# Kernel tuning notes

Measured on AMD Instinct MI355X. Metric: run time of the kernel, lower is better.

Reference implementation:

```python
import jax, jax.numpy as jnp
import numpy as np

B, N, DIN, D, E, STEP = 4, 1024, 256, 256, 5, 5


def setup_inputs() -> dict:
    key = jax.random.key(0)
    ks = jax.random.split(key, 14)
    s = 0.02  # weight init scale
    inp = {
        "node_features": jax.random.normal(ks[0], (B, N, DIN), dtype=jnp.float32),
        # dense per-edge-type adjacency; scaled so messages stay in a sane range
        "adj_matrices": jax.random.uniform(ks[1], (B, E, N, N), dtype=jnp.float32) * (2.0 / N),
        "fc_in_w": jax.random.normal(ks[2], (D, DIN), dtype=jnp.float32) * s,
        "fc_in_b": jnp.zeros((D,), dtype=jnp.float32),
        "edge_w": jax.random.normal(ks[3], (E, D, D), dtype=jnp.float32) * s,
        "edge_b": jax.random.normal(ks[4], (E, D), dtype=jnp.float32) * s,
        "gru_w_ih": jax.random.normal(ks[5], (3 * D, D), dtype=jnp.float32) * s,
        "gru_w_hh": jax.random.normal(ks[6], (3 * D, D), dtype=jnp.float32) * s,
        "gru_b_ih": jnp.zeros((3 * D,), dtype=jnp.float32),
        "gru_b_hh": jnp.zeros((3 * D,), dtype=jnp.float32),
        "conv1_w": jax.random.normal(ks[7], (D, D), dtype=jnp.float32) * s,
        "conv1_b": jnp.zeros((D,), dtype=jnp.float32),
        "conv2_w": jax.random.normal(ks[8], (D, D), dtype=jnp.float32) * s,
        "conv2_b": jnp.zeros((D,), dtype=jnp.float32),
    }
    return inp


def _gru_cell(x, h, w_ih, w_hh, b_ih, b_hh):
    # torch GRUCell: gates ordered [r, z, n]
    gi = x @ w_ih.T + b_ih  # [B*N, 3D]
    gh = h @ w_hh.T + b_hh
    ir, iz, inn = jnp.split(gi, 3, axis=-1)
    hr, hz, hn = jnp.split(gh, 3, axis=-1)
    r = jax.nn.sigmoid(ir + hr)
    z = jax.nn.sigmoid(iz + hz)
    n = jnp.tanh(inn + r * hn)
    return (1.0 - z) * n + z * h


def reference(node_features, adj_matrices, fc_in_w, fc_in_b, edge_w, edge_b,
              gru_w_ih, gru_w_hh, gru_b_ih, gru_b_hh,
              conv1_w, conv1_b, conv2_w, conv2_b):
    h = node_features @ fc_in_w.T + fc_in_b  # [B, N, D]
    sum_edge_b = jnp.sum(edge_b, axis=0)  # accumulated biases over edge types
    for _ in range(STEP):
        # messages per edge type: adj_e @ h  -> [B, E, N, D]
        msgs = jnp.einsum('benm,bmd->bend', adj_matrices, h)
        # per-edge-type linear (y = x @ W_e.T) then accumulate over edge types
        acc = jnp.einsum('bend,ekd->bnk', msgs, edge_w) + sum_edge_b  # [B, N, D]
        h = _gru_cell(acc, h, gru_w_ih, gru_w_hh, gru_b_ih, gru_b_hh)
    node_states = h  # [B, N, D]
    # conv1d with kernel_size=1 over node axis == per-node linear on channels
    attn_weights = jax.nn.sigmoid(node_states @ conv1_w.T + conv1_b)  # [B, N, D]
    feats = jnp.tanh(node_states @ conv2_w.T + conv2_b)  # [B, N, D]
    graph_embedding = jnp.sum(attn_weights * feats, axis=1)  # sum over nodes -> [B, D]
    attn_map = jnp.mean(attn_weights, axis=2)  # mean over channels -> [B, N]
    return (graph_embedding, node_states, attn_map)
```

## Files before the change

kernel.cpp:

```cpp
#include <hip/hip_runtime.h>
#include <hip/hip_bf16.h>
#include <cstdint>


typedef __attribute__((ext_vector_type(8))) short bf16x8;
typedef __attribute__((ext_vector_type(4))) float f32x4;

__device__ __forceinline__ float bf2f(__hip_bfloat16 x) { return __bfloat162float(x); }
__device__ __forceinline__ __hip_bfloat16 f2bf(float x) { return __float2bfloat16(x); }
__device__ __forceinline__ short f2bs(float x) {
  __hip_bfloat16 h = __float2bfloat16(x);
  return *reinterpret_cast<short*>(&h);
}
__device__ __forceinline__ float s2f(short x) {
  __hip_bfloat16 h = *reinterpret_cast<__hip_bfloat16*>(&x);
  return __bfloat162float(h);
}

__device__ __forceinline__ bf16x8 ld8_ext(const void* base, long off, bool f32) {
  if (f32) {
    const float* p = (const float*)base + off;
    bf16x8 r;
#pragma unroll
    for (int i = 0; i < 8; ++i) r[i] = f2bs(p[i]);
    return r;
  }
  return *(const bf16x8*)((const __hip_bfloat16*)base + off);
}

__device__ __forceinline__ bf16x8 ld8_sum5(const __hip_bfloat16* part, int row, int k) {
  const long base = (long)row * 256 + (long)(row >> 10) * 1048576 + k;
  float s[8] = {0.f, 0.f, 0.f, 0.f, 0.f, 0.f, 0.f, 0.f};
#pragma unroll
  for (int e = 0; e < 5; ++e) {
    bf16x8 v = *(const bf16x8*)(part + base + e * 262144);
#pragma unroll
    for (int j = 0; j < 8; ++j) s[j] += s2f(v[j]);
  }
  bf16x8 r;
#pragma unroll
  for (int j = 0; j < 8; ++j) r[j] = f2bs(s[j]);
  return r;
}

__global__ void detect_dtype(const uint32_t* __restrict__ raw, int* __restrict__ flag) {
  __shared__ int cnt;
  if (threadIdx.x == 0) cnt = 0;
  __syncthreads();
  int c = 0;
  for (int i = threadIdx.x; i < 512; i += 256) {
    uint32_t byte = (raw[i] >> 8) & 0xFF;
    if (byte >= 0x28 && byte <= 0x40) ++c;
  }
  atomicAdd(&cnt, c);
  __syncthreads();
  if (threadIdx.x == 0) *flag = (cnt < 300) ? 1 : 0;
}

__global__ void prep_pool(const void* fcb, const void* bih, const void* bhh,
                          const void* c1b, const void* c2b, const void* edgeb,
                          const int* __restrict__ flag,
                          float* __restrict__ pool, float* __restrict__ ge,
                          float* __restrict__ am32) {
  const bool f32 = (*flag != 0);
  for (int t = threadIdx.x; t < 2560; t += 256) {
    const void* p; int i;
    if (t < 256)       { p = fcb;  i = t; }
    else if (t < 1024) { p = bih;  i = t - 256; }
    else if (t < 1792) { p = bhh;  i = t - 1024; }
    else if (t < 2048) { p = c1b;  i = t - 1792; }
    else if (t < 2304) { p = c2b;  i = t - 2048; }
    else {
      int k = t - 2304; float s = 0.f;
      for (int e = 0; e < 5; ++e)
        s += f32 ? ((const float*)edgeb)[e * 256 + k]
                 : bf2f(((const __hip_bfloat16*)edgeb)[e * 256 + k]);
      pool[t] = s; continue;
    }
    pool[t] = f32 ? ((const float*)p)[i] : bf2f(((const __hip_bfloat16*)p)[i]);
  }
  for (int t = threadIdx.x; t < 1024; t += 256) ge[t] = 0.f;
  for (int t = threadIdx.x; t < 4096; t += 256) am32[t] = 0.f;
}

__global__ void bias_gi_k(const float* __restrict__ pool,
                          const __hip_bfloat16* __restrict__ wih,
                          float* __restrict__ out) {
  const int n = blockIdx.x * 256 + threadIdx.x;
  if (n >= 768) return;
  float s = pool[256 + n];
  for (int k = 0; k < 256; ++k) s += pool[2304 + k] * bf2f(wih[n * 256 + k]);
  out[n] = s;
}

__global__ void wcvt_all(const void* fcw, const void* edw, const void* wih,
                         const void* whh, const void* c1w, const void* c2w,
                         const int* __restrict__ flag, __hip_bfloat16* __restrict__ dst) {
  const bool f32 = (*flag != 0);
  const int i = blockIdx.x * 256 + threadIdx.x;
  const void* src; int off;
  if      (i < 65536)  { src = fcw; off = i; }
  else if (i < 393216) { src = edw; off = i - 65536; }
  else if (i < 589824) { src = wih; off = i - 393216; }
  else if (i < 786432) { src = whh; off = i - 589824; }
  else if (i < 851968) { src = c1w; off = i - 786432; }
  else                 { src = c2w; off = i - 851968; }
  dst[i] = f32 ? f2bf(((const float*)src)[off])
               : ((const __hip_bfloat16*)src)[off];
}

__global__ void adj_cvt(const void* __restrict__ src, const int* __restrict__ flag,
                        __hip_bfloat16* __restrict__ dst) {
  const bool f32 = (*flag != 0);
  const long i = ((long)blockIdx.x * 256 + threadIdx.x) * 8;
  bf16x8 r;
  if (f32) {
    const float* p = (const float*)src + i;
#pragma unroll
    for (int j = 0; j < 8; ++j) r[j] = f2bs(p[j]);
  } else {
    r = *(const bf16x8*)((const __hip_bfloat16*)src + i);
  }
  *(bf16x8*)(dst + i) = r;
}

template<bool HAS_BIAS, bool DUAL>
__global__ __launch_bounds__(256)
void gemm_bt128(const __hip_bfloat16* __restrict__ A, const __hip_bfloat16* __restrict__ Bt,
                const float* __restrict__ bias, __hip_bfloat16* __restrict__ C,
                const __hip_bfloat16* __restrict__ A2, const __hip_bfloat16* __restrict__ Bt2,
                const float* __restrict__ bias2, __hip_bfloat16* __restrict__ C2,
                int K, int lda, int ldb, int ldc,
                long aBatch, int zdivA, int zmodA,
                long bBatch, int zdivB, int zmodB,
                long cBatch, int zdivC, int zSplit)
{
  __shared__ __align__(16) __hip_bfloat16 sA[128 * 64];
  __shared__ __align__(16) __hip_bfloat16 sB[64 * 64];
  const int t = threadIdx.x;
  const int w = t >> 6;
  const int l = t & 63;
  const int m0 = blockIdx.x * 128;
  const int n0 = blockIdx.y * 64;
  int z = blockIdx.z;

  const __hip_bfloat16* Au = A; const __hip_bfloat16* Btu = Bt;
  const float* biasu = bias; __hip_bfloat16* Cu = C;
  if (DUAL && z >= zSplit) { Au = A2; Btu = Bt2; biasu = bias2; Cu = C2; z -= zSplit; }

  const __hip_bfloat16* Ab = Au + (long)((z / zdivA) % zmodA) * aBatch;
  const __hip_bfloat16* Bb = Btu + (long)((z / zdivB) % zmodB) * bBatch;

  int sra[4], sca[4];
#pragma unroll
  for (int i = 0; i < 4; ++i) {
    const int p = t + 256 * i;
    sra[i] = p >> 3;
    sca[i] = (p & 7) ^ (sra[i] & 7);
  }
  const int p0 = t, p1 = t + 256;
  const int sr0 = p0 >> 3, sc0 = (p0 & 7) ^ (sr0 & 7);
  const int sr1 = p1 >> 3, sc1 = (p1 & 7) ^ (sr1 & 7);

  f32x4 acc[2][4];
#pragma unroll
  for (int i = 0; i < 2; ++i)
#pragma unroll
    for (int j = 0; j < 4; ++j) acc[i][j] = (f32x4){0.f, 0.f, 0.f, 0.f};

  const int r15 = l & 15;
  const int quad = l >> 4;

  for (int k0 = 0; k0 < K; k0 += 64) {
    bf16x8 av[4];
#pragma unroll
    for (int i = 0; i < 4; ++i)
      av[i] = *(const bf16x8*)(Ab + (long)(m0 + sra[i]) * lda + (k0 + sca[i] * 8));
    bf16x8 b0 = *(const bf16x8*)(Bb + (long)(n0 + sr0) * ldb + (k0 + sc0 * 8));
    bf16x8 b1 = *(const bf16x8*)(Bb + (long)(n0 + sr1) * ldb + (k0 + sc1 * 8));
    __syncthreads();
#pragma unroll
    for (int i = 0; i < 4; ++i) *(bf16x8*)(sA + (t + 256 * i) * 8) = av[i];
    *(bf16x8*)(sB + p0 * 8) = b0;
    *(bf16x8*)(sB + p1 * 8) = b1;
    __syncthreads();
#pragma unroll
    for (int ks = 0; ks < 2; ++ks) {
      const int cg = ks * 4 + quad;
      bf16x8 aF[2], bF[4];
#pragma unroll
      for (int mi = 0; mi < 2; ++mi) {
        const int row = mi * 64 + w * 16 + r15;
        aF[mi] = *(const bf16x8*)(sA + row * 64 + ((cg ^ (row & 7)) * 8));
      }
#pragma unroll
      for (int ni = 0; ni < 4; ++ni) {
        const int nrow = ni * 16 + r15;
        bF[ni] = *(const bf16x8*)(sB + nrow * 64 + ((cg ^ (nrow & 7)) * 8));
      }
#pragma unroll
      for (int mi = 0; mi < 2; ++mi)
#pragma unroll
        for (int ni = 0; ni < 4; ++ni)
          acc[mi][ni] = __builtin_amdgcn_mfma_f32_16x16x32_bf16(
              aF[mi], bF[ni], acc[mi][ni], 0, 0, 0);
    }
  }

  const long cOff = (long)(z / zdivC) * cBatch;
#pragma unroll
  for (int mi = 0; mi < 2; ++mi) {
#pragma unroll
    for (int ni = 0; ni < 4; ++ni) {
      const int n = n0 + ni * 16 + r15;
      float bv = 0.f;
      if (HAS_BIAS) bv = biasu[n];
#pragma unroll
      for (int r = 0; r < 4; ++r) {
        const int m = m0 + mi * 64 + w * 16 + quad * 4 + r;
        Cu[cOff + (long)m * ldc + n] = f2bf(acc[mi][ni][r] + bv);
      }
    }
  }
}

__global__ __launch_bounds__(256)
void part_gh(const __hip_bfloat16* __restrict__ adjb,
             const __hip_bfloat16* __restrict__ heT,
             __hip_bfloat16* __restrict__ part,
             const __hip_bfloat16* __restrict__ hbf,
             const __hip_bfloat16* __restrict__ whh,
             const float* __restrict__ bhh,
             __hip_bfloat16* __restrict__ gh)
{
  __shared__ __align__(16) __hip_bfloat16 sA[128 * 64];
  __shared__ __align__(16) __hip_bfloat16 sB[64 * 64];
  const int t = threadIdx.x;
  const int w = t >> 6;
  const int l = t & 63;
  const int bid = blockIdx.x;

  const __hip_bfloat16* Ab; const __hip_bfloat16* Bb;
  __hip_bfloat16* Cu; const float* biasu = nullptr;
  int K, lda, ldb, ldc, m0, n0;
  bool has_bias;
  if (bid < 640) {
    const int z = bid >> 5, rem = bid & 31;
    m0 = (rem & 7) * 128; n0 = (rem >> 3) * 64;
    Ab = adjb + (long)z * 1048576; lda = 1024; K = 1024;
    Bb = heT + (long)z * 262144;  ldb = 1024;
    Cu = part + (long)z * 262144; ldc = 256;
    has_bias = false;
  } else {
    const int idx = bid - 640;
    m0 = (idx & 31) * 128; n0 = (idx >> 5) * 64;
    Ab = hbf; lda = 256; K = 256;
    Bb = whh; ldb = 256;
    Cu = gh;  ldc = 768;
    biasu = bhh; has_bias = true;
  }

  int sra[4], sca[4];
#pragma unroll
  for (int i = 0; i < 4; ++i) {
    const int p = t + 256 * i;
    sra[i] = p >> 3;
    sca[i] = (p & 7) ^ (sra[i] & 7);
  }
  const int p0 = t, p1 = t + 256;
  const int sr0 = p0 >> 3, sc0 = (p0 & 7) ^ (sr0 & 7);
  const int sr1 = p1 >> 3, sc1 = (p1 & 7) ^ (sr1 & 7);

  f32x4 acc[2][4];
#pragma unroll
  for (int i = 0; i < 2; ++i)
#pragma unroll
    for (int j = 0; j < 4; ++j) acc[i][j] = (f32x4){0.f, 0.f, 0.f, 0.f};

  const int r15 = l & 15;
  const int quad = l >> 4;

  for (int k0 = 0; k0 < K; k0 += 64) {
    bf16x8 av[4];
#pragma unroll
    for (int i = 0; i < 4; ++i)
      av[i] = *(const bf16x8*)(Ab + (long)(m0 + sra[i]) * lda + (k0 + sca[i] * 8));
    bf16x8 b0 = *(const bf16x8*)(Bb + (long)(n0 + sr0) * ldb + (k0 + sc0 * 8));
    bf16x8 b1 = *(const bf16x8*)(Bb + (long)(n0 + sr1) * ldb + (k0 + sc1 * 8));
    __syncthreads();
#pragma unroll
    for (int i = 0; i < 4; ++i) *(bf16x8*)(sA + (t + 256 * i) * 8) = av[i];
    *(bf16x8*)(sB + p0 * 8) = b0;
    *(bf16x8*)(sB + p1 * 8) = b1;
    __syncthreads();
#pragma unroll
    for (int ks = 0; ks < 2; ++ks) {
      const int cg = ks * 4 + quad;
      bf16x8 aF[2], bF[4];
#pragma unroll
      for (int mi = 0; mi < 2; ++mi) {
        const int row = mi * 64 + w * 16 + r15;
        aF[mi] = *(const bf16x8*)(sA + row * 64 + ((cg ^ (row & 7)) * 8));
      }
#pragma unroll
      for (int ni = 0; ni < 4; ++ni) {
        const int nrow = ni * 16 + r15;
        bF[ni] = *(const bf16x8*)(sB + nrow * 64 + ((cg ^ (nrow & 7)) * 8));
      }
#pragma unroll
      for (int mi = 0; mi < 2; ++mi)
#pragma unroll
        for (int ni = 0; ni < 4; ++ni)
          acc[mi][ni] = __builtin_amdgcn_mfma_f32_16x16x32_bf16(
              aF[mi], bF[ni], acc[mi][ni], 0, 0, 0);
    }
  }

#pragma unroll
  for (int mi = 0; mi < 2; ++mi) {
#pragma unroll
    for (int ni = 0; ni < 4; ++ni) {
      const int n = n0 + ni * 16 + r15;
      const float bv = has_bias ? biasu[n] : 0.f;
#pragma unroll
      for (int r = 0; r < 4; ++r) {
        const int m = m0 + mi * 64 + w * 16 + quad * 4 + r;
        Cu[(long)m * ldc + n] = f2bf(acc[mi][ni][r] + bv);
      }
    }
  }
}

__global__ __launch_bounds__(256)
void gi_gate(const __hip_bfloat16* __restrict__ part,
             const __hip_bfloat16* __restrict__ wih,
             const float* __restrict__ biasgi,
             const __hip_bfloat16* __restrict__ gh,
             __hip_bfloat16* __restrict__ hbf,
             void* __restrict__ ns_out, const int* __restrict__ flag)
{
  __shared__ __align__(16) __hip_bfloat16 sA[64 * 64];
  __shared__ __align__(16) __hip_bfloat16 sB0[64 * 64];
  __shared__ __align__(16) __hip_bfloat16 sB1[64 * 64];
  __shared__ __align__(16) __hip_bfloat16 sB2[64 * 64];
  const int t = threadIdx.x;
  const int w = t >> 6;
  const int l = t & 63;
  const int m0 = (blockIdx.x & 63) * 64;
  const int n0 = (blockIdx.x >> 6) * 64;

  const int p0 = t, p1 = t + 256;
  const int sr0 = p0 >> 3, sc0 = (p0 & 7) ^ (sr0 & 7);
  const int sr1 = p1 >> 3, sc1 = (p1 & 7) ^ (sr1 & 7);

  f32x4 acc[3][4];
#pragma unroll
  for (int g = 0; g < 3; ++g)
#pragma unroll
    for (int j = 0; j < 4; ++j) acc[g][j] = (f32x4){0.f, 0.f, 0.f, 0.f};

  const int mrow = w * 16 + (l & 15);
  const int r15 = l & 15;
  const int quad = l >> 4;

  for (int k0 = 0; k0 < 256; k0 += 64) {
    bf16x8 a0 = ld8_sum5(part, m0 + sr0, k0 + sc0 * 8);
    bf16x8 a1 = ld8_sum5(part, m0 + sr1, k0 + sc1 * 8);
    bf16x8 bg[3][2];
#pragma unroll
    for (int g = 0; g < 3; ++g) {
      bg[g][0] = *(const bf16x8*)(wih + (long)(g * 256 + n0 + sr0) * 256 + (k0 + sc0 * 8));
      bg[g][1] = *(const bf16x8*)(wih + (long)(g * 256 + n0 + sr1) * 256 + (k0 + sc1 * 8));
    }
    __syncthreads();
    *(bf16x8*)(sA + p0 * 8) = a0;
    *(bf16x8*)(sA + p1 * 8) = a1;
    *(bf16x8*)(sB0 + p0 * 8) = bg[0][0]; *(bf16x8*)(sB0 + p1 * 8) = bg[0][1];
    *(bf16x8*)(sB1 + p0 * 8) = bg[1][0]; *(bf16x8*)(sB1 + p1 * 8) = bg[1][1];
    *(bf16x8*)(sB2 + p0 * 8) = bg[2][0]; *(bf16x8*)(sB2 + p1 * 8) = bg[2][1];
    __syncthreads();
#pragma unroll
    for (int ks = 0; ks < 2; ++ks) {
      const int cg = ks * 4 + quad;
      bf16x8 af = *(const bf16x8*)(sA + mrow * 64 + ((cg ^ (mrow & 7)) * 8));
#pragma unroll
      for (int t4 = 0; t4 < 4; ++t4) {
        const int nrow = t4 * 16 + r15;
        const int so = nrow * 64 + ((cg ^ (nrow & 7)) * 8);
        bf16x8 b0f = *(const bf16x8*)(sB0 + so);
        bf16x8 b1f = *(const bf16x8*)(sB1 + so);
        bf16x8 b2f = *(const bf16x8*)(sB2 + so);
        acc[0][t4] = __builtin_amdgcn_mfma_f32_16x16x32_bf16(af, b0f, acc[0][t4], 0, 0, 0);
        acc[1][t4] = __builtin_amdgcn_mfma_f32_16x16x32_bf16(af, b1f, acc[1][t4], 0, 0, 0);
        acc[2][t4] = __builtin_amdgcn_mfma_f32_16x16x32_bf16(af, b2f, acc[2][t4], 0, 0, 0);
      }
    }
  }

  const bool f32out = ns_out && (*flag != 0);
#pragma unroll
  for (int t4 = 0; t4 < 4; ++t4) {
    const int n = n0 + t4 * 16 + r15;
    const float bgr = biasgi[n];
    const float bgz = biasgi[256 + n];
    const float bgn = biasgi[512 + n];
#pragma unroll
    for (int r = 0; r < 4; ++r) {
      const int m = m0 + w * 16 + quad * 4 + r;
      const long gb = (long)m * 768;
      const float ir = acc[0][t4][r] + bgr;
      const float iz = acc[1][t4][r] + bgz;
      const float inn = acc[2][t4][r] + bgn;
      const float hr = bf2f(gh[gb + n]);
      const float hz = bf2f(gh[gb + 256 + n]);
      const float hn = bf2f(gh[gb + 512 + n]);
      const long hidx = (long)m * 256 + n;
      const float h = bf2f(hbf[hidx]);
      const float rr = 1.f / (1.f + __expf(-(ir + hr)));
      const float zz = 1.f / (1.f + __expf(-(iz + hz)));
      const float nn = tanhf(inn + rr * hn);
      const float hnew = (1.f - zz) * nn + zz * h;
      const __hip_bfloat16 hb = f2bf(hnew);
      hbf[hidx] = hb;
      if (ns_out) {
        if (f32out) ((float*)ns_out)[1024 + hidx] = hnew;
        else        ((__hip_bfloat16*)ns_out)[1024 + hidx] = hb;
      }
    }
  }
}

template<int OUT_MODE, bool HAS_BIAS, int A_MODE, bool DUAL>
__global__ __launch_bounds__(256)
void gemm_bt(const void* __restrict__ A, const __hip_bfloat16* __restrict__ Bt,
             const float* __restrict__ bias, void* __restrict__ Cp,
             const void* __restrict__ A2, const __hip_bfloat16* __restrict__ Bt2,
             const float* __restrict__ bias2, void* __restrict__ Cp2,
             const int* __restrict__ flag,
             int Kg, int ngrp, int lda, int ldb, int ldc,
             long aBatch, int zdivA, int zmodA,
             long bBatch, int zdivB, int zmodB,
             long cBatch, int zdivC, long aGrp, long bGrp, int zSplit)
{
  __shared__ __align__(16) __hip_bfloat16 sA[64 * 64];
  __shared__ __align__(16) __hip_bfloat16 sB[64 * 64];
  const bool af32 = (A_MODE == 1) ? (*flag != 0) : false;
  const int t = threadIdx.x;
  const int w = t >> 6;
  const int l = t & 63;
  const int m0 = blockIdx.x * 64;
  const int n0 = blockIdx.y * 64;
  int z = blockIdx.z;

  const void* Au = A; const __hip_bfloat16* Btu = Bt;
  const float* biasu = bias; void* Cpu = Cp;
  bool second = false;
  if (DUAL && z >= zSplit) {
    Au = A2; Btu = Bt2; biasu = bias2; Cpu = Cp2; z -= zSplit; second = true;
  }

  const long aOff = (long)((z / zdivA) % zmodA) * aBatch;
  const __hip_bfloat16* Bb = Btu + (long)((z / zdivB) % zmodB) * bBatch;

  const int p0 = t, p1 = t + 256;
  const int sr0 = p0 >> 3, sc0 = (p0 & 7) ^ (sr0 & 7);
  const int sr1 = p1 >> 3, sc1 = (p1 & 7) ^ (sr1 & 7);

  f32x4 acc[4];
#pragma unroll
  for (int i = 0; i < 4; ++i) acc[i] = (f32x4){0.f, 0.f, 0.f, 0.f};

  const int mrow = w * 16 + (l & 15);
  const int quad = l >> 4;

  for (int g = 0; g < ngrp; ++g) {
    const long aG = aOff + (long)g * aGrp;
    const __hip_bfloat16* Bg = Bb + (long)g * bGrp;
    for (int k0 = 0; k0 < Kg; k0 += 64) {
      bf16x8 a0, a1;
      if (A_MODE == 2 && !second) {
        a0 = ld8_sum5((const __hip_bfloat16*)Au, m0 + sr0, k0 + sc0 * 8);
        a1 = ld8_sum5((const __hip_bfloat16*)Au, m0 + sr1, k0 + sc1 * 8);
      } else if (A_MODE == 1) {
        a0 = ld8_ext(Au, aG + (long)(m0 + sr0) * lda + (k0 + sc0 * 8), af32);
        a1 = ld8_ext(Au, aG + (long)(m0 + sr1) * lda + (k0 + sc1 * 8), af32);
      } else {
        const __hip_bfloat16* Ab = (const __hip_bfloat16*)Au;
        a0 = *(const bf16x8*)(Ab + aG + (long)(m0 + sr0) * lda + (k0 + sc0 * 8));
        a1 = *(const bf16x8*)(Ab + aG + (long)(m0 + sr1) * lda + (k0 + sc1 * 8));
      }
      bf16x8 b0 = *(const bf16x8*)(Bg + (long)(n0 + sr0) * ldb + (k0 + sc0 * 8));
      bf16x8 b1 = *(const bf16x8*)(Bg + (long)(n0 + sr1) * ldb + (k0 + sc1 * 8));
      __syncthreads();
      *(bf16x8*)(sA + p0 * 8) = a0;
      *(bf16x8*)(sA + p1 * 8) = a1;
      *(bf16x8*)(sB + p0 * 8) = b0;
      *(bf16x8*)(sB + p1 * 8) = b1;
      __syncthreads();
#pragma unroll
      for (int ks = 0; ks < 2; ++ks) {
        const int cg = ks * 4 + quad;
        bf16x8 af = *(const bf16x8*)(sA + mrow * 64 + ((cg ^ (mrow & 7)) * 8));
#pragma unroll
        for (int t4 = 0; t4 < 4; ++t4) {
          const int nrow = t4 * 16 + (l & 15);
          bf16x8 bfr = *(const bf16x8*)(sB + nrow * 64 + ((cg ^ (nrow & 7)) * 8));
          acc[t4] = __builtin_amdgcn_mfma_f32_16x16x32_bf16(af, bfr, acc[t4], 0, 0, 0);
        }
      }
    }
  }

  const long cOff = (long)(z / zdivC) * cBatch;
#pragma unroll
  for (int t4 = 0; t4 < 4; ++t4) {
    const int n = n0 + t4 * 16 + (l & 15);
    float bv = 0.f;
    if (HAS_BIAS) bv = biasu[n];
#pragma unroll
    for (int r = 0; r < 4; ++r) {
      const int m = m0 + w * 16 + quad * 4 + r;
      const float v = acc[t4][r] + bv;
      if (OUT_MODE == 0)
        ((__hip_bfloat16*)Cpu)[cOff + (long)m * ldc + n] = f2bf(v);
      else
        ((float*)Cpu)[cOff + (long)m * ldc + n] = v;
    }
  }
}

__global__ void gru_gate8(const __hip_bfloat16* __restrict__ gi,
                          const __hip_bfloat16* __restrict__ gh,
                          __hip_bfloat16* __restrict__ hbf,
                          void* __restrict__ ns_out, const int* __restrict__ flag)
{
  const int t = blockIdx.x * 256 + threadIdx.x;
  const int m = t >> 5;
  const int k = (t & 31) * 8;
  const long gb = (long)m * 768 + k;
  bf16x8 vir = *(const bf16x8*)(gi + gb);
  bf16x8 viz = *(const bf16x8*)(gi + gb + 256);
  bf16x8 vin = *(const bf16x8*)(gi + gb + 512);
  bf16x8 vhr = *(const bf16x8*)(gh + gb);
  bf16x8 vhz = *(const bf16x8*)(gh + gb + 256);
  bf16x8 vhn = *(const bf16x8*)(gh + gb + 512);
  const long hidx = (long)m * 256 + k;
  bf16x8 vh = *(const bf16x8*)(hbf + hidx);
  bf16x8 out;
  float hf[8];
#pragma unroll
  for (int j = 0; j < 8; ++j) {
    const float r = 1.f / (1.f + __expf(-(s2f(vir[j]) + s2f(vhr[j]))));
    const float zz = 1.f / (1.f + __expf(-(s2f(viz[j]) + s2f(vhz[j]))));
    const float nn = tanhf(s2f(vin[j]) + r * s2f(vhn[j]));
    hf[j] = (1.f - zz) * nn + zz * s2f(vh[j]);
    out[j] = f2bs(hf[j]);
  }
  *(bf16x8*)(hbf + hidx) = out;
  if (ns_out) {
    if (*flag) {
      float* o = (float*)ns_out + 1024 + hidx;
#pragma unroll
      for (int j = 0; j < 8; ++j) o[j] = hf[j];
    } else {
      *(bf16x8*)((__hip_bfloat16*)ns_out + 1024 + hidx) = out;
    }
  }
}

__global__ __launch_bounds__(256)
void conv_fused(const __hip_bfloat16* __restrict__ hbf,
                const __hip_bfloat16* __restrict__ c1w,
                const __hip_bfloat16* __restrict__ c2w,
                const float* __restrict__ pool,
                float* __restrict__ geg, float* __restrict__ am32)
{
  __shared__ __align__(16) __hip_bfloat16 sA[64 * 64];
  __shared__ __align__(16) __hip_bfloat16 sB1[64 * 64];
  __shared__ __align__(16) __hip_bfloat16 sB2[64 * 64];
  __shared__ float sge[64];
  __shared__ float sam[64];
  const int t = threadIdx.x, w = t >> 6, l = t & 63;
  const int m0 = blockIdx.x * 64, n0 = blockIdx.y * 64;
  if (t < 64) { sge[t] = 0.f; sam[t] = 0.f; }
  const int p0 = t, p1 = t + 256;
  const int sr0 = p0 >> 3, sc0 = (p0 & 7) ^ (sr0 & 7);
  const int sr1 = p1 >> 3, sc1 = (p1 & 7) ^ (sr1 & 7);
  f32x4 a1[4], a2[4];
#pragma unroll
  for (int i = 0; i < 4; ++i) { a1[i] = (f32x4){0,0,0,0}; a2[i] = (f32x4){0,0,0,0}; }
  const int mrow = w * 16 + (l & 15);
  const int quad = l >> 4;
  for (int k0 = 0; k0 < 256; k0 += 64) {
    bf16x8 va0 = *(const bf16x8*)(hbf + (long)(m0 + sr0) * 256 + (k0 + sc0 * 8));
    bf16x8 va1 = *(const bf16x8*)(hbf + (long)(m0 + sr1) * 256 + (k0 + sc1 * 8));
    bf16x8 vb0 = *(const bf16x8*)(c1w + (long)(n0 + sr0) * 256 + (k0 + sc0 * 8));
    bf16x8 vb1 = *(const bf16x8*)(c1w + (long)(n0 + sr1) * 256 + (k0 + sc1 * 8));
    bf16x8 vc0 = *(const bf16x8*)(c2w + (long)(n0 + sr0) * 256 + (k0 + sc0 * 8));
    bf16x8 vc1 = *(const bf16x8*)(c2w + (long)(n0 + sr1) * 256 + (k0 + sc1 * 8));
    __syncthreads();
    *(bf16x8*)(sA + p0 * 8) = va0;  *(bf16x8*)(sA + p1 * 8) = va1;
    *(bf16x8*)(sB1 + p0 * 8) = vb0; *(bf16x8*)(sB1 + p1 * 8) = vb1;
    *(bf16x8*)(sB2 + p0 * 8) = vc0; *(bf16x8*)(sB2 + p1 * 8) = vc1;
    __syncthreads();
#pragma unroll
    for (int ks = 0; ks < 2; ++ks) {
      const int cg = ks * 4 + quad;
      bf16x8 af = *(const bf16x8*)(sA + mrow * 64 + ((cg ^ (mrow & 7)) * 8));
#pragma unroll
      for (int t4 = 0; t4 < 4; ++t4) {
        const int nrow = t4 * 16 + (l & 15);
        bf16x8 b1f = *(const bf16x8*)(sB1 + nrow * 64 + ((cg ^ (nrow & 7)) * 8));
        bf16x8 b2f = *(const bf16x8*)(sB2 + nrow * 64 + ((cg ^ (nrow & 7)) * 8));
        a1[t4] = __builtin_amdgcn_mfma_f32_16x16x32_bf16(af, b1f, a1[t4], 0, 0, 0);
        a2[t4] = __builtin_amdgcn_mfma_f32_16x16x32_bf16(af, b2f, a2[t4], 0, 0, 0);
      }
    }
  }
  float asum[4] = {0.f, 0.f, 0.f, 0.f};
#pragma unroll
  for (int t4 = 0; t4 < 4; ++t4) {
    const int n = n0 + t4 * 16 + (l & 15);
    const float bb1 = pool[1792 + n], bb2 = pool[2048 + n];
    float g = 0.f;
#pragma unroll
    for (int r = 0; r < 4; ++r) {
      const float av = 1.f / (1.f + __expf(-(a1[t4][r] + bb1)));
      const float fv = tanhf(a2[t4][r] + bb2);
      g += av * fv;
      asum[r] += av;
    }
    atomicAdd(&sge[t4 * 16 + (l & 15)], g);
  }
#pragma unroll
  for (int r = 0; r < 4; ++r) atomicAdd(&sam[w * 16 + quad * 4 + r], asum[r]);
  __syncthreads();
  if (t < 64) atomicAdd(&geg[(m0 >> 10) * 256 + n0 + t], sge[t]);
  else if (t < 128) atomicAdd(&am32[m0 + (t - 64)], sam[t - 64]);
}

__global__ void finish_out(const float* __restrict__ ge, const float* __restrict__ am32,
                           void* __restrict__ dout, const int* __restrict__ flag)
{
  const int t = blockIdx.x * 256 + threadIdx.x;
  const bool f32 = (*flag != 0);
  if (t < 1024) {
    if (f32) ((float*)dout)[t] = ge[t];
    else     ((__hip_bfloat16*)dout)[t] = f2bf(ge[t]);
  } else {
    const float v = am32[t - 1024] * (1.f / 256.f);
    if (f32) ((float*)dout)[1049600 + t - 1024] = v;
    else     ((__hip_bfloat16*)dout)[1049600 + t - 1024] = f2bf(v);
  }
}

extern "C" void kernel_launch(void* const* d_in, const int* in_sizes, int n_in,
                              void* d_out, int out_size, void* d_ws, size_t ws_size,
                              hipStream_t stream) {
  (void)in_sizes; (void)n_in; (void)out_size;
  const void* node_f = d_in[0];
  const void* adj    = d_in[1];
  const void* fc_w   = d_in[2];
  const void* fc_b   = d_in[3];
  const void* edge_w = d_in[4];
  const void* edge_b = d_in[5];
  const void* w_ih   = d_in[6];
  const void* w_hh   = d_in[7];
  const void* b_ih   = d_in[8];
  const void* b_hh   = d_in[9];
  const void* c1w    = d_in[10];
  const void* c1b    = d_in[11];
  const void* c2w    = d_in[12];
  const void* c2b    = d_in[13];

  char* ws = (char*)d_ws;
  const size_t MB = (size_t)1 << 20;
  int*            flag = (int*)(ws);
  float*          bp   = (float*)(ws + 256);
  float*          ge   = (float*)(ws + 14336);
  float*          am32 = (float*)(ws + 18432);
  __hip_bfloat16* wbf  = (__hip_bfloat16*)(ws + 34816);
  __hip_bfloat16* hbf  = (__hip_bfloat16*)(ws + 1869824);
  char*           S    = ws + 3966976;
  __hip_bfloat16* heT  = (__hip_bfloat16*)(S);
  __hip_bfloat16* part = (__hip_bfloat16*)(S + 10 * MB);
  __hip_bfloat16* gi   = (__hip_bfloat16*)(S + 20 * MB);
  __hip_bfloat16* gh   = (__hip_bfloat16*)(S + 26 * MB);
  __hip_bfloat16* adjb = (__hip_bfloat16*)(ws + 40 * MB);

  const bool has_split = ws_size >= 38 * MB;
  const bool has_adjb  = ws_size >= 81 * MB;

  detect_dtype<<<1, 256, 0, stream>>>((const uint32_t*)adj, flag);
  prep_pool<<<1, 256, 0, stream>>>(fc_b, b_ih, b_hh, c1b, c2b, edge_b, flag, bp, ge, am32);
  wcvt_all<<<3584, 256, 0, stream>>>(fc_w, edge_w, w_ih, w_hh, c1w, c2w, flag, wbf);
  bias_gi_k<<<3, 256, 0, stream>>>(bp, wbf + 393216, bp + 2560);
  if (has_adjb) adj_cvt<<<10240, 256, 0, stream>>>(adj, flag, adjb);

  gemm_bt<0, true, 1, false><<<dim3(64, 4, 1), 256, 0, stream>>>(
      node_f, wbf + 0, bp + 0, hbf, nullptr, nullptr, nullptr, nullptr, flag,
      256, 1, 256, 256, 256, 0, 1, 1, 0, 1, 1, 0, 1, 0, 0, 0);

  for (int s = 0; s < 5; ++s) {
    if (has_adjb) {
      gemm_bt128<false, false><<<dim3(2, 16, 20), 256, 0, stream>>>(
          wbf + 65536, hbf, nullptr, heT, nullptr, nullptr, nullptr, nullptr,
          256, 256, 256, 1024,
          65536, 1, 5,
          262144, 5, 4,
          262144, 1, 0);
      part_gh<<<1024, 256, 0, stream>>>(adjb, heT, part,
                                        hbf, wbf + 589824, bp + 1024, gh);
      gi_gate<<<256, 256, 0, stream>>>(part, wbf + 393216, bp + 2560, gh, hbf,
                                       (s == 4) ? d_out : nullptr, flag);
    } else if (has_split) {
      gemm_bt<0, false, 0, false><<<dim3(4, 16, 20), 256, 0, stream>>>(
          wbf + 65536, hbf, nullptr, heT, nullptr, nullptr, nullptr, nullptr, flag,
          256, 1, 256, 256, 1024,
          65536, 1, 5, 262144, 5, 4,
          262144, 1, 0, 0, 0);
      gemm_bt<0, false, 1, false><<<dim3(16, 4, 20), 256, 0, stream>>>(
          adj, heT, nullptr, part, nullptr, nullptr, nullptr, nullptr, flag,
          1024, 1, 1024, 1024, 256,
          1048576, 1, 20, 262144, 1, 20,
          262144, 1, 0, 0, 0);
      gemm_bt<0, true, 2, true><<<dim3(64, 12, 2), 256, 0, stream>>>(
          part, wbf + 393216, bp + 2560, gi,
          hbf,  wbf + 589824, bp + 1024, gh, flag,
          256, 1, 256, 256, 768, 0, 1, 1, 0, 1, 1, 0, 1, 0, 0, 1);
      gru_gate8<<<512, 256, 0, stream>>>(gi, gh, hbf,
                                         (s == 4) ? d_out : nullptr, flag);
    } else {
      gemm_bt<0, false, 0, false><<<dim3(4, 16, 20), 256, 0, stream>>>(
          wbf + 65536, hbf, nullptr, heT, nullptr, nullptr, nullptr, nullptr, flag,
          256, 1, 256, 256, 1024,
          65536, 1, 5, 262144, 5, 4,
          262144, 1, 0, 0, 0);
      gemm_bt<0, true, 1, false><<<dim3(16, 4, 4), 256, 0, stream>>>(
          adj, heT, bp + 2304, part, nullptr, nullptr, nullptr, nullptr, flag,
          1024, 5, 1024, 1024, 256,
          (long)5 * 1048576, 1, 4, (long)5 * 262144, 1, 4,
          262144, 1, 1048576, 262144, 0);
      gemm_bt<0, true, 0, true><<<dim3(64, 12, 2), 256, 0, stream>>>(
          part, wbf + 393216, bp + 256, gi,
          hbf,  wbf + 589824, bp + 1024, gh, flag,
          256, 1, 256, 256, 768, 0, 1, 1, 0, 1, 1, 0, 1, 0, 0, 1);
      gru_gate8<<<512, 256, 0, stream>>>(gi, gh, hbf,
                                         (s == 4) ? d_out : nullptr, flag);
    }
  }

  conv_fused<<<dim3(64, 4), 256, 0, stream>>>(hbf, wbf + 786432, wbf + 851968,
                                              bp, ge, am32);
  finish_out<<<20, 256, 0, stream>>>(ge, am32, d_out, flag);
}
```

Before: 432.8 us.

## Fold edge weights into GRU input weights and drop per-step edge GEMM

Reassociates the message path: instead of computing h@W_e^T per edge type each step, the code multiplies adjacency by h directly (msgs per edge) and folds W_ih into the edge weights once up front (V_e = W_ih·W_e), so the GRU input GEMM consumes all five edge messages over a K of 1280. This removes one GEMM launch per step and writes a transposed copy of h from the gate epilogue so the adjacency GEMM can read it directly. In exchange the gi GEMM has five times larger K and the adjacency GEMM output buffer now holds per-edge messages. A simple register prefetch of the next k-tile is added to the gi loop.

```diff
diff --git a/kernel.cpp b/kernel.cpp
--- a/kernel.cpp
+++ b/kernel.cpp
@@ -95,9 +95,21 @@
 
 __global__ void wcvt_all(const void* fcw, const void* edw, const void* wih,
                          const void* whh, const void* c1w, const void* c2w,
-                         const int* __restrict__ flag, __hip_bfloat16* __restrict__ dst) {
+                         const int* __restrict__ flag, __hip_bfloat16* __restrict__ dst,
+                         __hip_bfloat16* __restrict__ ewT) {
   const bool f32 = (*flag != 0);
   const int i = blockIdx.x * 256 + threadIdx.x;
+  if (i >= 917504) {
+    if (!ewT) return;
+    const int j = i - 917504;
+    const int e = j >> 16;
+    const int r = j & 65535;
+    const int d = r >> 8, k = r & 255;
+    const int off = e * 65536 + k * 256 + d;
+    ewT[j] = f32 ? f2bf(((const float*)edw)[off])
+                 : ((const __hip_bfloat16*)edw)[off];
+    return;
+  }
   const void* src; int off;
   if      (i < 65536)  { src = fcw; off = i; }
   else if (i < 393216) { src = edw; off = i - 65536; }
@@ -124,114 +136,14 @@
   *(bf16x8*)(dst + i) = r;
 }
 
-template<bool HAS_BIAS, bool DUAL>
 __global__ __launch_bounds__(256)
-void gemm_bt128(const __hip_bfloat16* __restrict__ A, const __hip_bfloat16* __restrict__ Bt,
-                const float* __restrict__ bias, __hip_bfloat16* __restrict__ C,
-                const __hip_bfloat16* __restrict__ A2, const __hip_bfloat16* __restrict__ Bt2,
-                const float* __restrict__ bias2, __hip_bfloat16* __restrict__ C2,
-                int K, int lda, int ldb, int ldc,
-                long aBatch, int zdivA, int zmodA,
-                long bBatch, int zdivB, int zmodB,
-                long cBatch, int zdivC, int zSplit)
-{
-  __shared__ __align__(16) __hip_bfloat16 sA[128 * 64];
-  __shared__ __align__(16) __hip_bfloat16 sB[64 * 64];
-  const int t = threadIdx.x;
-  const int w = t >> 6;
-  const int l = t & 63;
-  const int m0 = blockIdx.x * 128;
-  const int n0 = blockIdx.y * 64;
-  int z = blockIdx.z;
-
-  const __hip_bfloat16* Au = A; const __hip_bfloat16* Btu = Bt;
-  const float* biasu = bias; __hip_bfloat16* Cu = C;
-  if (DUAL && z >= zSplit) { Au = A2; Btu = Bt2; biasu = bias2; Cu = C2; z -= zSplit; }
-
-  const __hip_bfloat16* Ab = Au + (long)((z / zdivA) % zmodA) * aBatch;
-  const __hip_bfloat16* Bb = Btu + (long)((z / zdivB) % zmodB) * bBatch;
-
-  int sra[4], sca[4];
-#pragma unroll
-  for (int i = 0; i < 4; ++i) {
-    const int p = t + 256 * i;
-    sra[i] = p >> 3;
-    sca[i] = (p & 7) ^ (sra[i] & 7);
-  }
-  const int p0 = t, p1 = t + 256;
-  const int sr0 = p0 >> 3, sc0 = (p0 & 7) ^ (sr0 & 7);
-  const int sr1 = p1 >> 3, sc1 = (p1 & 7) ^ (sr1 & 7);
-
-  f32x4 acc[2][4];
-#pragma unroll
-  for (int i = 0; i < 2; ++i)
-#pragma unroll
-    for (int j = 0; j < 4; ++j) acc[i][j] = (f32x4){0.f, 0.f, 0.f, 0.f};
-
-  const int r15 = l & 15;
-  const int quad = l >> 4;
-
-  for (int k0 = 0; k0 < K; k0 += 64) {
-    bf16x8 av[4];
-#pragma unroll
-    for (int i = 0; i < 4; ++i)
-      av[i] = *(const bf16x8*)(Ab + (long)(m0 + sra[i]) * lda + (k0 + sca[i] * 8));
-    bf16x8 b0 = *(const bf16x8*)(Bb + (long)(n0 + sr0) * ldb + (k0 + sc0 * 8));
-    bf16x8 b1 = *(const bf16x8*)(Bb + (long)(n0 + sr1) * ldb + (k0 + sc1 * 8));
-    __syncthreads();
-#pragma unroll
-    for (int i = 0; i < 4; ++i) *(bf16x8*)(sA + (t + 256 * i) * 8) = av[i];
-    *(bf16x8*)(sB + p0 * 8) = b0;
-    *(bf16x8*)(sB + p1 * 8) = b1;
-    __syncthreads();
-#pragma unroll
-    for (int ks = 0; ks < 2; ++ks) {
-      const int cg = ks * 4 + quad;
-      bf16x8 aF[2], bF[4];
-#pragma unroll
-      for (int mi = 0; mi < 2; ++mi) {
-        const int row = mi * 64 + w * 16 + r15;
-        aF[mi] = *(const bf16x8*)(sA + row * 64 + ((cg ^ (row & 7)) * 8));
-      }
-#pragma unroll
-      for (int ni = 0; ni < 4; ++ni) {
-        const int nrow = ni * 16 + r15;
-        bF[ni] = *(const bf16x8*)(sB + nrow * 64 + ((cg ^ (nrow & 7)) * 8));
-      }
-#pragma unroll
-      for (int mi = 0; mi < 2; ++mi)
-#pragma unroll
-        for (int ni = 0; ni < 4; ++ni)
-          acc[mi][ni] = __builtin_amdgcn_mfma_f32_16x16x32_bf16(
-              aF[mi], bF[ni], acc[mi][ni], 0, 0, 0);
-    }
-  }
-
-  const long cOff = (long)(z / zdivC) * cBatch;
-#pragma unroll
-  for (int mi = 0; mi < 2; ++mi) {
-#pragma unroll
-    for (int ni = 0; ni < 4; ++ni) {
-      const int n = n0 + ni * 16 + r15;
-      float bv = 0.f;
-      if (HAS_BIAS) bv = biasu[n];
-#pragma unroll
-      for (int r = 0; r < 4; ++r) {
-        const int m = m0 + mi * 64 + w * 16 + quad * 4 + r;
-        Cu[cOff + (long)m * ldc + n] = f2bf(acc[mi][ni][r] + bv);
-      }
-    }
-  }
-}
-
-__global__ __launch_bounds__(256)
-void part_gh(const __hip_bfloat16* __restrict__ adjb,
-             const __hip_bfloat16* __restrict__ heT,
-             __hip_bfloat16* __restrict__ part,
-             const __hip_bfloat16* __restrict__ hbf,
-             const __hip_bfloat16* __restrict__ whh,
-             const float* __restrict__ bhh,
-             __hip_bfloat16* __restrict__ gh)
+void ms_gh(const __hip_bfloat16* __restrict__ adjb,
+           const __hip_bfloat16* __restrict__ hT,
+           __hip_bfloat16* __restrict__ ms,
+           const __hip_bfloat16* __restrict__ hbf,
+           const __hip_bfloat16* __restrict__ whh,
+           const float* __restrict__ bhh,
+           __hip_bfloat16* __restrict__ gh)
 {
   __shared__ __align__(16) __hip_bfloat16 sA[128 * 64];
   __shared__ __align__(16) __hip_bfloat16 sB[64 * 64];
@@ -248,8 +160,8 @@
     const int z = bid >> 5, rem = bid & 31;
     m0 = (rem & 7) * 128; n0 = (rem >> 3) * 64;
     Ab = adjb + (long)z * 1048576; lda = 1024; K = 1024;
-    Bb = heT + (long)z * 262144;  ldb = 1024;
-    Cu = part + (long)z * 262144; ldc = 256;
+    Bb = hT + (long)(z / 5) * 262144; ldb = 1024;
+    Cu = ms + (long)z * 262144; ldc = 256;
     has_bias = false;
   } else {
     const int idx = bid - 640;
@@ -332,12 +244,13 @@
 }
 
 __global__ __launch_bounds__(256)
-void gi_gate(const __hip_bfloat16* __restrict__ part,
-             const __hip_bfloat16* __restrict__ wih,
-             const float* __restrict__ biasgi,
-             const __hip_bfloat16* __restrict__ gh,
-             __hip_bfloat16* __restrict__ hbf,
-             void* __restrict__ ns_out, const int* __restrict__ flag)
+void gi_gate3(const __hip_bfloat16* __restrict__ ms,
+              const __hip_bfloat16* __restrict__ V,
+              const float* __restrict__ biasgi,
+              const __hip_bfloat16* __restrict__ gh,
+              __hip_bfloat16* __restrict__ hbf,
+              __hip_bfloat16* __restrict__ hT,
+              void* __restrict__ ns_out, const int* __restrict__ flag)
 {
   __shared__ __align__(16) __hip_bfloat16 sA[64 * 64];
   __shared__ __align__(16) __hip_bfloat16 sB0[64 * 64];
@@ -353,6 +266,8 @@
   const int sr0 = p0 >> 3, sc0 = (p0 & 7) ^ (sr0 & 7);
   const int sr1 = p1 >> 3, sc1 = (p1 & 7) ^ (sr1 & 7);
 
+  const __hip_bfloat16* msB = ms + (long)(m0 >> 10) * 1310720 + (long)(m0 & 1023) * 256;
+
   f32x4 acc[3][4];
 #pragma unroll
   for (int g = 0; g < 3; ++g)
@@ -363,22 +278,39 @@
   const int r15 = l & 15;
   const int quad = l >> 4;
 
-  for (int k0 = 0; k0 < 256; k0 += 64) {
-    bf16x8 a0 = ld8_sum5(part, m0 + sr0, k0 + sc0 * 8);
-    bf16x8 a1 = ld8_sum5(part, m0 + sr1, k0 + sc1 * 8);
-    bf16x8 bg[3][2];
-#pragma unroll
-    for (int g = 0; g < 3; ++g) {
-      bg[g][0] = *(const bf16x8*)(wih + (long)(g * 256 + n0 + sr0) * 256 + (k0 + sc0 * 8));
-      bg[g][1] = *(const bf16x8*)(wih + (long)(g * 256 + n0 + sr1) * 256 + (k0 + sc1 * 8));
-    }
+  bf16x8 a0, a1, bg0a, bg0b, bg1a, bg1b, bg2a, bg2b;
+  {
+    const int e = 0, dd = 0;
+    a0 = *(const bf16x8*)(msB + e * 262144 + sr0 * 256 + (dd + sc0 * 8));
+    a1 = *(const bf16x8*)(msB + e * 262144 + sr1 * 256 + (dd + sc1 * 8));
+    bg0a = *(const bf16x8*)(V + (long)e * 196608 + (0 * 256 + n0 + sr0) * 256 + (dd + sc0 * 8));
+    bg0b = *(const bf16x8*)(V + (long)e * 196608 + (0 * 256 + n0 + sr1) * 256 + (dd + sc1 * 8));
+    bg1a = *(const bf16x8*)(V + (long)e * 196608 + (1 * 256 + n0 + sr0) * 256 + (dd + sc0 * 8));
+    bg1b = *(const bf16x8*)(V + (long)e * 196608 + (1 * 256 + n0 + sr1) * 256 + (dd + sc1 * 8));
+    bg2a = *(const bf16x8*)(V + (long)e * 196608 + (2 * 256 + n0 + sr0) * 256 + (dd + sc0 * 8));
+    bg2b = *(const bf16x8*)(V + (long)e * 196608 + (2 * 256 + n0 + sr1) * 256 + (dd + sc1 * 8));
+  }
+
+  for (int ki = 0; ki < 20; ++ki) {
     __syncthreads();
     *(bf16x8*)(sA + p0 * 8) = a0;
     *(bf16x8*)(sA + p1 * 8) = a1;
-    *(bf16x8*)(sB0 + p0 * 8) = bg[0][0]; *(bf16x8*)(sB0 + p1 * 8) = bg[0][1];
-    *(bf16x8*)(sB1 + p0 * 8) = bg[1][0]; *(bf16x8*)(sB1 + p1 * 8) = bg[1][1];
-    *(bf16x8*)(sB2 + p0 * 8) = bg[2][0]; *(bf16x8*)(sB2 + p1 * 8) = bg[2][1];
+    *(bf16x8*)(sB0 + p0 * 8) = bg0a; *(bf16x8*)(sB0 + p1 * 8) = bg0b;
+    *(bf16x8*)(sB1 + p0 * 8) = bg1a; *(bf16x8*)(sB1 + p1 * 8) = bg1b;
+    *(bf16x8*)(sB2 + p0 * 8) = bg2a; *(bf16x8*)(sB2 + p1 * 8) = bg2b;
     __syncthreads();
+    if (ki < 19) {
+      const int k0 = (ki + 1) * 64;
+      const int e = k0 >> 8, dd = k0 & 255;
+      a0 = *(const bf16x8*)(msB + e * 262144 + sr0 * 256 + (dd + sc0 * 8));
+      a1 = *(const bf16x8*)(msB + e * 262144 + sr1 * 256 + (dd + sc1 * 8));
+      bg0a = *(const bf16x8*)(V + (long)e * 196608 + (0 * 256 + n0 + sr0) * 256 + (dd + sc0 * 8));
+      bg0b = *(const bf16x8*)(V + (long)e * 196608 + (0 * 256 + n0 + sr1) * 256 + (dd + sc1 * 8));
+      bg1a = *(const bf16x8*)(V + (long)e * 196608 + (1 * 256 + n0 + sr0) * 256 + (dd + sc0 * 8));
+      bg1b = *(const bf16x8*)(V + (long)e * 196608 + (1 * 256 + n0 + sr1) * 256 + (dd + sc1 * 8));
+      bg2a = *(const bf16x8*)(V + (long)e * 196608 + (2 * 256 + n0 + sr0) * 256 + (dd + sc0 * 8));
+      bg2b = *(const bf16x8*)(V + (long)e * 196608 + (2 * 256 + n0 + sr1) * 256 + (dd + sc1 * 8));
+    }
 #pragma unroll
     for (int ks = 0; ks < 2; ++ks) {
       const int cg = ks * 4 + quad;
@@ -422,6 +354,7 @@
       const float hnew = (1.f - zz) * nn + zz * h;
       const __hip_bfloat16 hb = f2bf(hnew);
       hbf[hidx] = hb;
+      hT[(long)(m >> 10) * 262144 + (long)n * 1024 + (m & 1023)] = hb;
       if (ns_out) {
         if (f32out) ((float*)ns_out)[1024 + hidx] = hnew;
         else        ((__hip_bfloat16*)ns_out)[1024 + hidx] = hb;
@@ -521,10 +454,14 @@
     for (int r = 0; r < 4; ++r) {
       const int m = m0 + w * 16 + quad * 4 + r;
       const float v = acc[t4][r] + bv;
-      if (OUT_MODE == 0)
-        ((__hip_bfloat16*)Cpu)[cOff + (long)m * ldc + n] = f2bf(v);
-      else
+      if (OUT_MODE == 1) {
         ((float*)Cpu)[cOff + (long)m * ldc + n] = v;
+      } else {
+        const __hip_bfloat16 hb = f2bf(v);
+        ((__hip_bfloat16*)Cpu)[cOff + (long)m * ldc + n] = hb;
+        if (OUT_MODE == 2)
+          ((__hip_bfloat16*)Cp2)[(long)(m >> 10) * 262144 + (long)n * 1024 + (m & 1023)] = hb;
+      }
     }
   }
 }
@@ -683,7 +620,10 @@
   __hip_bfloat16* hbf  = (__hip_bfloat16*)(ws + 1869824);
   char*           S    = ws + 3966976;
   __hip_bfloat16* heT  = (__hip_bfloat16*)(S);
-  __hip_bfloat16* part = (__hip_bfloat16*)(S + 10 * MB);
+  __hip_bfloat16* ms   = (__hip_bfloat16*)(S + 10 * MB);
+  __hip_bfloat16* Vbuf = (__hip_bfloat16*)(S + 20 * MB);
+  __hip_bfloat16* ewT  = (__hip_bfloat16*)(S + 22 * MB);
+  __hip_bfloat16* hT   = (__hip_bfloat16*)(S + 23 * MB);
   __hip_bfloat16* gi   = (__hip_bfloat16*)(S + 20 * MB);
   __hip_bfloat16* gh   = (__hip_bfloat16*)(S + 26 * MB);
   __hip_bfloat16* adjb = (__hip_bfloat16*)(ws + 40 * MB);
@@ -693,26 +633,32 @@
 
   detect_dtype<<<1, 256, 0, stream>>>((const uint32_t*)adj, flag);
   prep_pool<<<1, 256, 0, stream>>>(fc_b, b_ih, b_hh, c1b, c2b, edge_b, flag, bp, ge, am32);
-  wcvt_all<<<3584, 256, 0, stream>>>(fc_w, edge_w, w_ih, w_hh, c1w, c2w, flag, wbf);
+  wcvt_all<<<4864, 256, 0, stream>>>(fc_w, edge_w, w_ih, w_hh, c1w, c2w, flag, wbf,
+                                     has_adjb ? ewT : nullptr);
   bias_gi_k<<<3, 256, 0, stream>>>(bp, wbf + 393216, bp + 2560);
-  if (has_adjb) adj_cvt<<<10240, 256, 0, stream>>>(adj, flag, adjb);
-
-  gemm_bt<0, true, 1, false><<<dim3(64, 4, 1), 256, 0, stream>>>(
-      node_f, wbf + 0, bp + 0, hbf, nullptr, nullptr, nullptr, nullptr, flag,
-      256, 1, 256, 256, 256, 0, 1, 1, 0, 1, 1, 0, 1, 0, 0, 0);
+  if (has_adjb) {
+    adj_cvt<<<10240, 256, 0, stream>>>(adj, flag, adjb);
+    gemm_bt<0, false, 0, false><<<dim3(12, 4, 5), 256, 0, stream>>>(
+        wbf + 393216, ewT, nullptr, Vbuf, nullptr, nullptr, nullptr, nullptr, flag,
+        256, 1, 256, 256, 256,
+        0, 1, 1,
+        65536, 1, 5,
+        196608, 1, 0, 0, 0);
+    gemm_bt<2, true, 1, false><<<dim3(64, 4, 1), 256, 0, stream>>>(
+        node_f, wbf + 0, bp + 0, hbf, nullptr, nullptr, nullptr, hT, flag,
+        256, 1, 256, 256, 256, 0, 1, 1, 0, 1, 1, 0, 1, 0, 0, 0);
+  } else {
+    gemm_bt<0, true, 1, false><<<dim3(64, 4, 1), 256, 0, stream>>>(
+        node_f, wbf + 0, bp + 0, hbf, nullptr, nullptr, nullptr, nullptr, flag,
+        256, 1, 256, 256, 256, 0, 1, 1, 0, 1, 1, 0, 1, 0, 0, 0);
+  }
 
   for (int s = 0; s < 5; ++s) {
     if (has_adjb) {
-      gemm_bt128<false, false><<<dim3(2, 16, 20), 256, 0, stream>>>(
-          wbf + 65536, hbf, nullptr, heT, nullptr, nullptr, nullptr, nullptr,
-          256, 256, 256, 1024,
-          65536, 1, 5,
-          262144, 5, 4,
-          262144, 1, 0);
-      part_gh<<<1024, 256, 0, stream>>>(adjb, heT, part,
-                                        hbf, wbf + 589824, bp + 1024, gh);
-      gi_gate<<<256, 256, 0, stream>>>(part, wbf + 393216, bp + 2560, gh, hbf,
-                                       (s == 4) ? d_out : nullptr, flag);
+      ms_gh<<<1024, 256, 0, stream>>>(adjb, hT, ms,
+                                      hbf, wbf + 589824, bp + 1024, gh);
+      gi_gate3<<<256, 256, 0, stream>>>(ms, Vbuf, bp + 2560, gh, hbf, hT,
+                                        (s == 4) ? d_out : nullptr, flag);
     } else if (has_split) {
       gemm_bt<0, false, 0, false><<<dim3(4, 16, 20), 256, 0, stream>>>(
           wbf + 65536, hbf, nullptr, heT, nullptr, nullptr, nullptr, nullptr, flag,
@@ -720,12 +666,12 @@
           65536, 1, 5, 262144, 5, 4,
           262144, 1, 0, 0, 0);
       gemm_bt<0, false, 1, false><<<dim3(16, 4, 20), 256, 0, stream>>>(
-          adj, heT, nullptr, part, nullptr, nullptr, nullptr, nullptr, flag,
+          adj, heT, nullptr, ms, nullptr, nullptr, nullptr, nullptr, flag,
           1024, 1, 1024, 1024, 256,
           1048576, 1, 20, 262144, 1, 20,
           262144, 1, 0, 0, 0);
       gemm_bt<0, true, 2, true><<<dim3(64, 12, 2), 256, 0, stream>>>(
-          part, wbf + 393216, bp + 2560, gi,
+          ms, wbf + 393216, bp + 2560, gi,
           hbf,  wbf + 589824, bp + 1024, gh, flag,
           256, 1, 256, 256, 768, 0, 1, 1, 0, 1, 1, 0, 1, 0, 0, 1);
       gru_gate8<<<512, 256, 0, stream>>>(gi, gh, hbf,
@@ -737,12 +683,12 @@
           65536, 1, 5, 262144, 5, 4,
           262144, 1, 0, 0, 0);
       gemm_bt<0, true, 1, false><<<dim3(16, 4, 4), 256, 0, stream>>>(
-          adj, heT, bp + 2304, part, nullptr, nullptr, nullptr, nullptr, flag,
+          adj, heT, bp + 2304, ms, nullptr, nullptr, nullptr, nullptr, flag,
           1024, 5, 1024, 1024, 256,
           (long)5 * 1048576, 1, 4, (long)5 * 262144, 1, 4,
           262144, 1, 1048576, 262144, 0);
       gemm_bt<0, true, 0, true><<<dim3(64, 12, 2), 256, 0, stream>>>(
-          part, wbf + 393216, bp + 256, gi,
+          ms, wbf + 393216, bp + 256, gi,
           hbf,  wbf + 589824, bp + 1024, gh, flag,
           256, 1, 256, 256, 768, 0, 1, 1, 0, 1, 1, 0, 1, 0, 0, 1);
       gru_gate8<<<512, 256, 0, stream>>>(gi, gh, hbf,
```

After: 461.3 us. +6.6%, slower.
